# Optimization experiments

Hardware: AMD Instinct MI355X
Metric: run time of the kernel (lower is better)

## Reference

```python
import jax, jax.numpy as jnp
import numpy as np

B, S, D = 2, 2048, 2048
KVH, QPG, HD = 8, 4, 64          # kv heads, q heads per group, head size
THETA = 1024.0
PARTIAL = 0.5
SOFT_CAP = 50.0
EPS = 1e-5


def setup_inputs() -> dict:
    key = jax.random.key(0)
    ks = jax.random.split(key, 8)
    scale = 0.02
    return {
        "x": jax.random.normal(ks[0], (B, S, D), jnp.float32),
        "wq": jax.random.normal(ks[1], (KVH, QPG, HD, D), jnp.float32) * scale,
        "wk": jax.random.normal(ks[2], (KVH, HD, D), jnp.float32) * scale,
        "wv": jax.random.normal(ks[3], (KVH, HD, D), jnp.float32) * scale,
        "wo": jax.random.normal(ks[4], (D, KVH, QPG, HD), jnp.float32) * scale,
        "qn_w": jnp.ones((HD,), jnp.float32),
        "kn_w": jnp.ones((HD,), jnp.float32),
        "pos_ids": jnp.arange(S, dtype=jnp.int32),
    }


def _rms_norm(t, w):
    var = jnp.mean(jnp.square(t), axis=-1, keepdims=True)
    return t * jax.lax.rsqrt(var + EPS) * w


def _rope_tables(pos_ids):
    half = HD // 2
    rotated_size = int(HD * PARTIAL)
    inv_freq = 1.0 / THETA ** (jnp.arange(0, 2 * half, 2, dtype=jnp.float32) / rotated_size)
    inv_freq = jnp.where(jnp.arange(half) < rotated_size // 2, inv_freq, 0.0)
    freqs = pos_ids.astype(jnp.float32)[:, None] * inv_freq[None, :]   # [S, half]
    emb = jnp.concatenate([freqs, freqs], axis=-1)                      # [S, HD]
    return jnp.cos(emb), jnp.sin(emb)


def _apply_rope(t, cos, sin):
    # t: [..., S, HD]; rotate_half: (x1, x2) -> (-x2, x1)
    half = HD // 2
    x1, x2 = t[..., :half], t[..., half:]
    rot = jnp.concatenate([-x2, x1], axis=-1)
    return t * cos + rot * sin


def reference(x, wq, wk, wv, wo, qn_w, kn_w, pos_ids):
    # QKV projections (GQA)
    q = jnp.einsum("bsd,gphd->bgpsh", x, wq)   # [B,KVH,QPG,S,HD]
    k = jnp.einsum("bsd,ghd->bgsh", x, wk)      # [B,KVH,S,HD]
    v = jnp.einsum("bsd,ghd->bgsh", x, wv)

    # QK-norm (RMS over head dim)
    q = _rms_norm(q, qn_w)
    k = _rms_norm(k, kn_w)

    # partial RoPE
    cos, sin = _rope_tables(pos_ids)            # [S, HD]
    q = _apply_rope(q, cos, sin).astype(x.dtype)
    k = _apply_rope(k, cos, sin).astype(x.dtype)

    # attention in fp32 (upcast_attn) with soft cap and causal mask
    scale = 1.0 / jnp.sqrt(jnp.float32(HD))
    scores = jnp.einsum("bgpsh,bgth->bgpst", q.astype(jnp.float32), k.astype(jnp.float32)) * scale
    scores = SOFT_CAP * jnp.tanh(scores / SOFT_CAP)
    causal = pos_ids[:, None] >= pos_ids[None, :]                    # [S, S]
    scores = jnp.where(causal, scores, jnp.finfo(jnp.float32).min)
    probs = jax.nn.softmax(scores, axis=-1)
    attn = jnp.einsum("bgpst,bgth->bgpsh", probs, v.astype(jnp.float32)).astype(x.dtype)

    # output projection (flatten kv_head x q_heads_per_group -> heads)
    out = jnp.einsum("bgpsh,dgph->bsd", attn, wo)
    return out
```

## Files before the change

### kernel.cpp

```cpp
#include <hip/hip_runtime.h>
#include <stdint.h>

#define S_LEN   2048
#define D_MODEL 2048
#define N_KVH   8
#define N_QPG   4
#define N_HD    64

typedef __attribute__((ext_vector_type(8))) short  short8;
typedef __attribute__((ext_vector_type(4))) short  short4v;
typedef __attribute__((ext_vector_type(4))) float  float4v;

__device__ __forceinline__ unsigned short f2bf(float x) {
    unsigned int u = __float_as_uint(x);
    u = (u + 0x7fffu + ((u >> 16) & 1u)) >> 16;
    return (unsigned short)u;
}

__device__ __forceinline__ void gload_lds16(const unsigned short* g, unsigned short* l) {
    __builtin_amdgcn_global_load_lds((const __attribute__((address_space(1))) unsigned int*)g,
                                     (__attribute__((address_space(3))) unsigned int*)l,
                                     16, 0, 0);
}

__device__ __forceinline__ short8 lds_read8(const unsigned short* p) {
    union { short8 s8; short4v s4[2]; } u;
    u.s4[0] = *(const short4v*)p;
    u.s4[1] = *(const short4v*)(p + 4);
    return u.s8;
}

__global__ __launch_bounds__(256) void cvt_all(const float* __restrict__ x,
                                               const float* __restrict__ wq,
                                               const float* __restrict__ wk,
                                               const float* __restrict__ wv,
                                               const float* __restrict__ wo,
                                               unsigned short* __restrict__ xb,
                                               unsigned short* __restrict__ wqb,
                                               unsigned short* __restrict__ wkb,
                                               unsigned short* __restrict__ wvb,
                                               unsigned short* __restrict__ wob) {
    size_t i = (size_t)blockIdx.x * 256 + threadIdx.x;
    const float* src; unsigned short* dst; size_t off;
    if      (i < 1048576) { src = x;  dst = xb;  off = i; }
    else if (i < 1572864) { src = wq; dst = wqb; off = i - 1048576; }
    else if (i < 1703936) { src = wk; dst = wkb; off = i - 1572864; }
    else if (i < 1835008) { src = wv; dst = wvb; off = i - 1703936; }
    else                  { src = wo; dst = wob; off = i - 1835008; }
    const float4* p = (const float4*)src + off * 2;
    float4 a = p[0], b = p[1];
    union { unsigned short us[8]; uint4 v; } u;
    u.us[0] = f2bf(a.x); u.us[1] = f2bf(a.y); u.us[2] = f2bf(a.z); u.us[3] = f2bf(a.w);
    u.us[4] = f2bf(b.x); u.us[5] = f2bf(b.y); u.us[6] = f2bf(b.z); u.us[7] = f2bf(b.w);
    ((uint4*)dst)[off] = u.v;
}

#define EPI_OUT 0
#define EPI_Q   1

template<int EPI>
__global__ __launch_bounds__(256)
void gemm_bt(const unsigned short* __restrict__ A,
             const unsigned short* __restrict__ B,
             void* __restrict__ C,
             const float* __restrict__ normw,
             int M, int N, int K)
{
    __shared__ __align__(16) unsigned short Alds[128 * 32];
    __shared__ __align__(16) unsigned short Blds[128 * 32];

    const int tid  = threadIdx.x;
    const int lane = tid & 63;
    const int wave = tid >> 6;
    const int quad = lane >> 4;
    const int l15  = lane & 15;
    const int m0 = blockIdx.x * 128;
    const int n0 = blockIdx.y * 128;
    const int wm = (wave >> 1) * 64;
    const int wn = (wave & 1) * 64;

    float4v acc[4][4];
#pragma unroll
    for (int i = 0; i < 4; i++)
#pragma unroll
        for (int j = 0; j < 4; j++) acc[i][j] = (float4v){0.f, 0.f, 0.f, 0.f};

    const int j0 = wave * 2;
    const int lr = lane >> 2;
    const int lc = (lane & 3) * 8;
    const unsigned short* Ag = A + (size_t)(m0 + j0 * 16 + lr) * K + lc;
    const unsigned short* Bg = B + (size_t)(n0 + j0 * 16 + lr) * K + lc;
    unsigned short* Al = Alds + j0 * 512;
    unsigned short* Bl = Blds + j0 * 512;

    for (int k0 = 0; k0 < K; k0 += 32) {
        __syncthreads();
        gload_lds16(Ag + k0,          Al);
        gload_lds16(Ag + 16 * K + k0, Al + 512);
        gload_lds16(Bg + k0,          Bl);
        gload_lds16(Bg + 16 * K + k0, Bl + 512);
        __syncthreads();

        short8 af[4], bf[4];
#pragma unroll
        for (int mt = 0; mt < 4; mt++)
            af[mt] = *(const short8*)(Alds + (wm + mt * 16 + l15) * 32 + quad * 8);
#pragma unroll
        for (int nt = 0; nt < 4; nt++)
            bf[nt] = *(const short8*)(Blds + (wn + nt * 16 + l15) * 32 + quad * 8);
#pragma unroll
        for (int mt = 0; mt < 4; mt++)
#pragma unroll
            for (int nt = 0; nt < 4; nt++)
                acc[mt][nt] = __builtin_amdgcn_mfma_f32_16x16x32_bf16(af[mt], bf[nt], acc[mt][nt], 0, 0, 0);
    }

    const int nb = n0 + wn;
#pragma unroll
    for (int mt = 0; mt < 4; mt++) {
#pragma unroll
        for (int r = 0; r < 4; r++) {
            const int m = m0 + wm + mt * 16 + quad * 4 + r;
            if constexpr (EPI == EPI_OUT) {
#pragma unroll
                for (int nt = 0; nt < 4; nt++) {
                    int n = nb + nt * 16 + l15;
                    ((float*)C)[(size_t)m * N + n] = acc[mt][nt][r];
                }
            } else {
                float v0 = acc[mt][0][r], v1 = acc[mt][1][r], v2 = acc[mt][2][r], v3 = acc[mt][3][r];
                float s2 = v0 * v0 + v1 * v1 + v2 * v2 + v3 * v3;
#pragma unroll
                for (int off = 1; off < 16; off <<= 1) s2 += __shfl_xor(s2, off, 64);
                float rs = rsqrtf(s2 * (1.0f / 64.0f) + 1e-5f);
                float nv0 = v0 * rs * normw[0 * 16 + l15];
                float nv1 = v1 * rs * normw[1 * 16 + l15];
                float nv2 = v2 * rs * normw[2 * 16 + l15];
                float nv3 = v3 * rs * normw[3 * 16 + l15];
                const int bidx = m >> 11, s = m & 2047;
                float ang = (float)s * exp2f(-0.625f * (float)l15);
                float sn, cs;
                __sincosf(ang, &sn, &cs);
                float o0 = nv0 * cs - nv2 * sn;
                float o2 = nv2 * cs + nv0 * sn;
                const int g = nb >> 8, p = (nb >> 6) & 3;
                unsigned short* dst = (unsigned short*)C +
                    ((((size_t)bidx * N_KVH + g) * N_QPG + p) * S_LEN + s) * N_HD;
                dst[0 * 16 + l15] = f2bf(o0);
                dst[1 * 16 + l15] = f2bf(nv1);
                dst[2 * 16 + l15] = f2bf(o2);
                dst[3 * 16 + l15] = f2bf(nv3);
            }
        }
    }
}

__global__ __launch_bounds__(256)
void gemm_kv(const unsigned short* __restrict__ xb,
             const unsigned short* __restrict__ wkb,
             const unsigned short* __restrict__ wvb,
             unsigned short* __restrict__ kout,
             unsigned short* __restrict__ vtout,
             const float* __restrict__ knw)
{
    __shared__ __align__(16) unsigned short Alds[128 * 32];
    __shared__ __align__(16) unsigned short Blds[128 * 32];

    const int tid  = threadIdx.x;
    const int lane = tid & 63;
    const int wave = tid >> 6;
    const int quad = lane >> 4;
    const int l15  = lane & 15;
    const int bx = blockIdx.x, by = blockIdx.y;
    const bool isK = (by < 4);
    const unsigned short* A = isK ? xb  : wvb;
    const unsigned short* B = isK ? wkb : xb;
    const int m0 = isK ? bx * 128 : (by - 4) * 128;
    const int n0 = isK ? by * 128 : bx * 128;
    const int K = 2048;
    const int wm = (wave >> 1) * 64;
    const int wn = (wave & 1) * 64;

    float4v acc[4][4];
#pragma unroll
    for (int i = 0; i < 4; i++)
#pragma unroll
        for (int j = 0; j < 4; j++) acc[i][j] = (float4v){0.f, 0.f, 0.f, 0.f};

    const int j0 = wave * 2;
    const int lr = lane >> 2;
    const int lc = (lane & 3) * 8;
    const unsigned short* Ag = A + (size_t)(m0 + j0 * 16 + lr) * K + lc;
    const unsigned short* Bg = B + (size_t)(n0 + j0 * 16 + lr) * K + lc;
    unsigned short* Al = Alds + j0 * 512;
    unsigned short* Bl = Blds + j0 * 512;

    for (int k0 = 0; k0 < K; k0 += 32) {
        __syncthreads();
        gload_lds16(Ag + k0,          Al);
        gload_lds16(Ag + 16 * K + k0, Al + 512);
        gload_lds16(Bg + k0,          Bl);
        gload_lds16(Bg + 16 * K + k0, Bl + 512);
        __syncthreads();

        short8 af[4], bf[4];
#pragma unroll
        for (int mt = 0; mt < 4; mt++)
            af[mt] = *(const short8*)(Alds + (wm + mt * 16 + l15) * 32 + quad * 8);
#pragma unroll
        for (int nt = 0; nt < 4; nt++)
            bf[nt] = *(const short8*)(Blds + (wn + nt * 16 + l15) * 32 + quad * 8);
#pragma unroll
        for (int mt = 0; mt < 4; mt++)
#pragma unroll
            for (int nt = 0; nt < 4; nt++)
                acc[mt][nt] = __builtin_amdgcn_mfma_f32_16x16x32_bf16(af[mt], bf[nt], acc[mt][nt], 0, 0, 0);
    }

    const int nb = n0 + wn;
#pragma unroll
    for (int mt = 0; mt < 4; mt++) {
#pragma unroll
        for (int r = 0; r < 4; r++) {
            const int m = m0 + wm + mt * 16 + quad * 4 + r;
            if (isK) {
                float v0 = acc[mt][0][r], v1 = acc[mt][1][r], v2 = acc[mt][2][r], v3 = acc[mt][3][r];
                float s2 = v0 * v0 + v1 * v1 + v2 * v2 + v3 * v3;
#pragma unroll
                for (int off = 1; off < 16; off <<= 1) s2 += __shfl_xor(s2, off, 64);
                float rs = rsqrtf(s2 * (1.0f / 64.0f) + 1e-5f);
                float nv0 = v0 * rs * knw[0 * 16 + l15];
                float nv1 = v1 * rs * knw[1 * 16 + l15];
                float nv2 = v2 * rs * knw[2 * 16 + l15];
                float nv3 = v3 * rs * knw[3 * 16 + l15];
                const int bidx = m >> 11, s = m & 2047;
                float ang = (float)s * exp2f(-0.625f * (float)l15);
                float sn, cs;
                __sincosf(ang, &sn, &cs);
                float o0 = nv0 * cs - nv2 * sn;
                float o2 = nv2 * cs + nv0 * sn;
                const int g = nb >> 6;
                unsigned short* dst = kout +
                    (((size_t)bidx * N_KVH + g) * S_LEN + s) * N_HD;
                dst[0 * 16 + l15] = f2bf(o0);
                dst[1 * 16 + l15] = f2bf(nv1);
                dst[2 * 16 + l15] = f2bf(o2);
                dst[3 * 16 + l15] = f2bf(nv3);
            } else {
#pragma unroll
                for (int nt = 0; nt < 4; nt++) {
                    int n = nb + nt * 16 + l15;
                    vtout[((size_t)(n >> 11) * 512 + m) * 2048 + (n & 2047)] =
                        f2bf(acc[mt][nt][r]);
                }
            }
        }
    }
}

#define PSTRIDE 68

__global__ __launch_bounds__(256)
void attn_kernel(const unsigned short* __restrict__ Q,
                 const unsigned short* __restrict__ Kb,
                 const unsigned short* __restrict__ Vt,
                 unsigned short* __restrict__ O)
{
    __shared__ __align__(16) unsigned short Kf[8 * 512];
    __shared__ __align__(16) unsigned short Vf[8 * 512];
    __shared__ __align__(16) unsigned short Plds[4 * 32 * PSTRIDE];

    const int tid  = threadIdx.x;
    const int lane = tid & 63;
    const int w    = tid >> 6;
    const int quad = lane >> 4;
    const int l15  = lane & 15;
    const int lhi  = lane >> 4;
    const int qt = 63 - blockIdx.x;
    const int qrow0 = qt * 32;
    const int bg = blockIdx.y;
    const int b = bg >> 3, g = bg & 7;

    const unsigned short* qbase  = Q  + (((size_t)b * N_KVH + g) * N_QPG + w) * S_LEN * N_HD;
    const unsigned short* kbase  = Kb + ((size_t)b * N_KVH + g) * S_LEN * N_HD;
    const unsigned short* vtbase = Vt + ((size_t)b * N_KVH + g) * (size_t)N_HD * S_LEN;

    const unsigned short* sptr[4];
    unsigned short*       ldst[4];
    int                   step[4];
#pragma unroll
    for (int j = 0; j < 4; j++) {
        int ri = w * 4 + j;
        int isV = ri >> 3, rr = ri & 7, nt = rr >> 1, ks = rr & 1;
        if (isV) {
            sptr[j] = vtbase + (size_t)(nt * 16 + l15) * S_LEN + ks * 32 + lhi * 8;
            step[j] = 64;
            ldst[j] = Vf + rr * 512;
        } else {
            sptr[j] = kbase + (size_t)(nt * 16 + l15) * N_HD + ks * 32 + lhi * 8;
            step[j] = 64 * N_HD;
            ldst[j] = Kf + rr * 512;
        }
    }

    unsigned short* Pw = Plds + w * (32 * PSTRIDE);

    short8 qf[2][2];
#pragma unroll
    for (int mt = 0; mt < 2; mt++)
#pragma unroll
        for (int ks = 0; ks < 2; ks++)
            qf[mt][ks] = *(const short8*)(qbase + (size_t)(qrow0 + mt * 16 + l15) * N_HD + ks * 32 + quad * 8);

    float4v o_acc[2][4];
#pragma unroll
    for (int mt = 0; mt < 2; mt++)
#pragma unroll
        for (int nt = 0; nt < 4; nt++) o_acc[mt][nt] = (float4v){0.f, 0.f, 0.f, 0.f};
    float rsum[2][4];
#pragma unroll
    for (int mt = 0; mt < 2; mt++)
#pragma unroll
        for (int r = 0; r < 4; r++) rsum[mt][r] = 0.f;

    const int ktend = qrow0 >> 6;
    for (int kt = 0; kt <= ktend; kt++) {
        __syncthreads();
#pragma unroll
        for (int j = 0; j < 4; j++)
            gload_lds16(sptr[j] + (size_t)kt * step[j], ldst[j]);
        __syncthreads();

        float4v s_acc[2][4];
#pragma unroll
        for (int mt = 0; mt < 2; mt++)
#pragma unroll
            for (int nt = 0; nt < 4; nt++) s_acc[mt][nt] = (float4v){0.f, 0.f, 0.f, 0.f};
#pragma unroll
        for (int ks = 0; ks < 2; ks++) {
            short8 kfr[4];
#pragma unroll
            for (int nt = 0; nt < 4; nt++)
                kfr[nt] = *(const short8*)(Kf + (nt * 2 + ks) * 512 + lane * 8);
#pragma unroll
            for (int mt = 0; mt < 2; mt++)
#pragma unroll
                for (int nt = 0; nt < 4; nt++)
                    s_acc[mt][nt] = __builtin_amdgcn_mfma_f32_16x16x32_bf16(qf[mt][ks], kfr[nt], s_acc[mt][nt], 0, 0, 0);
        }

        const bool diag = (kt == ktend);
#pragma unroll
        for (int mt = 0; mt < 2; mt++) {
#pragma unroll
            for (int r = 0; r < 4; r++) {
                const int s_q  = qrow0 + mt * 16 + quad * 4 + r;
                const int prow = (mt * 16 + quad * 4 + r) * PSTRIDE;
#pragma unroll
                for (int nt = 0; nt < 4; nt++) {
                    float a = s_acc[mt][nt][r];
                    float z = a * 2.5e-3f;
                    float t = fmaf(z * z, -0.33333334f, 1.0f);
                    float p = __builtin_amdgcn_exp2f(
                        fmaf(a * 0.18033688f, t, -72.13475204f));
                    if (diag) {
                        int s_k = kt * 64 + nt * 16 + l15;
                        p = (s_k <= s_q) ? p : 0.0f;
                    }
                    rsum[mt][r] += p;
                    Pw[prow + nt * 16 + l15] =
                        (unsigned short)((__float_as_uint(p) + 0x8000u) >> 16);
                }
            }
        }

#pragma unroll
        for (int ks = 0; ks < 2; ks++) {
            short8 pf[2], vfr[4];
#pragma unroll
            for (int mt = 0; mt < 2; mt++)
                pf[mt] = lds_read8(Pw + (mt * 16 + l15) * PSTRIDE + ks * 32 + quad * 8);
#pragma unroll
            for (int nt = 0; nt < 4; nt++)
                vfr[nt] = *(const short8*)(Vf + (nt * 2 + ks) * 512 + lane * 8);
#pragma unroll
            for (int mt = 0; mt < 2; mt++)
#pragma unroll
                for (int nt = 0; nt < 4; nt++)
                    o_acc[mt][nt] = __builtin_amdgcn_mfma_f32_16x16x32_bf16(pf[mt], vfr[nt], o_acc[mt][nt], 0, 0, 0);
        }
    }

#pragma unroll
    for (int mt = 0; mt < 2; mt++) {
#pragma unroll
        for (int r = 0; r < 4; r++) {
            float s = rsum[mt][r];
            s += __shfl_xor(s, 1, 64);
            s += __shfl_xor(s, 2, 64);
            s += __shfl_xor(s, 4, 64);
            s += __shfl_xor(s, 8, 64);
            float inv = 1.0f / s;
            int s_q = qrow0 + mt * 16 + quad * 4 + r;
            size_t rowoff = ((size_t)(b * S_LEN + s_q)) * D_MODEL + (g * N_QPG + w) * N_HD;
#pragma unroll
            for (int nt = 0; nt < 4; nt++)
                O[rowoff + nt * 16 + l15] = f2bf(o_acc[mt][nt][r] * inv);
        }
    }
}

extern "C" void kernel_launch(void* const* d_in, const int* in_sizes, int n_in,
                              void* d_out, int out_size, void* d_ws, size_t ws_size,
                              hipStream_t stream)
{
    const float* x    = (const float*)d_in[0];
    const float* wq   = (const float*)d_in[1];
    const float* wk   = (const float*)d_in[2];
    const float* wv   = (const float*)d_in[3];
    const float* wo   = (const float*)d_in[4];
    const float* qn_w = (const float*)d_in[5];
    const float* kn_w = (const float*)d_in[6];

    char* ws = (char*)d_ws;
    unsigned short* xb  = (unsigned short*)(ws + 0);
    unsigned short* wqb = (unsigned short*)(ws + 16777216);
    unsigned short* wkb = (unsigned short*)(ws + 25165824);
    unsigned short* wvb = (unsigned short*)(ws + 27262976);
    unsigned short* wob = (unsigned short*)(ws + 29360128);
    unsigned short* qb  = (unsigned short*)(ws + 37748736);
    unsigned short* kb  = (unsigned short*)(ws + 54525952);
    unsigned short* vt  = (unsigned short*)(ws + 58720256);
    unsigned short* ab  = (unsigned short*)(ws + 62914560);

    cvt_all<<<dim3(9216), 256, 0, stream>>>(x, wq, wk, wv, wo, xb, wqb, wkb, wvb, wob);

    gemm_bt<EPI_Q><<<dim3(32, 16), 256, 0, stream>>>(xb, wqb, qb, qn_w, 4096, 2048, 2048);
    gemm_kv<<<dim3(32, 8), 256, 0, stream>>>(xb, wkb, wvb, kb, vt, kn_w);

    attn_kernel<<<dim3(64, 16), 256, 0, stream>>>(qb, kb, vt, ab);

    gemm_bt<EPI_OUT><<<dim3(32, 16), 256, 0, stream>>>(ab, wob, d_out, nullptr, 4096, 2048, 2048);
}
```

Baseline: 420.3 us.

## Pair causal query tiles per block and load K/V directly into registers

Each attention block now handles two query tiles, qx and 63-qx, so the causal work per block is balanced, and the grid is halved. The shared-memory K/V staging and its two block barriers per step are removed. Each wave now loads K and V fragments straight from global memory into registers and prefetches the next K tile. The soft-cap polynomial is refactored into one fewer multiply. The trade-off is that all four waves load the same K/V redundantly from global/L2 with no sharing through LDS, and register pressure rises.

```diff
diff --git a/kernel.cpp b/kernel.cpp
--- a/kernel.cpp
+++ b/kernel.cpp
@@ -266,8 +266,6 @@
                  const unsigned short* __restrict__ Vt,
                  unsigned short* __restrict__ O)
 {
-    __shared__ __align__(16) unsigned short Kf[8 * 512];
-    __shared__ __align__(16) unsigned short Vf[8 * 512];
     __shared__ __align__(16) unsigned short Plds[4 * 32 * PSTRIDE];
 
     const int tid  = threadIdx.x;
@@ -275,9 +273,7 @@
     const int w    = tid >> 6;
     const int quad = lane >> 4;
     const int l15  = lane & 15;
-    const int lhi  = lane >> 4;
-    const int qt = 63 - blockIdx.x;
-    const int qrow0 = qt * 32;
+    const int qx = blockIdx.x;
     const int bg = blockIdx.y;
     const int b = bg >> 3, g = bg & 7;
 
@@ -285,127 +281,122 @@
     const unsigned short* kbase  = Kb + ((size_t)b * N_KVH + g) * S_LEN * N_HD;
     const unsigned short* vtbase = Vt + ((size_t)b * N_KVH + g) * (size_t)N_HD * S_LEN;
 
-    const unsigned short* sptr[4];
-    unsigned short*       ldst[4];
-    int                   step[4];
-#pragma unroll
-    for (int j = 0; j < 4; j++) {
-        int ri = w * 4 + j;
-        int isV = ri >> 3, rr = ri & 7, nt = rr >> 1, ks = rr & 1;
-        if (isV) {
-            sptr[j] = vtbase + (size_t)(nt * 16 + l15) * S_LEN + ks * 32 + lhi * 8;
-            step[j] = 64;
-            ldst[j] = Vf + rr * 512;
-        } else {
-            sptr[j] = kbase + (size_t)(nt * 16 + l15) * N_HD + ks * 32 + lhi * 8;
-            step[j] = 64 * N_HD;
-            ldst[j] = Kf + rr * 512;
+    unsigned short* Pw = Plds + w * (32 * PSTRIDE);
+
+    for (int half = 0; half < 2; half++) {
+        const int qt = half ? (63 - qx) : qx;
+        const int qrow0 = qt * 32;
+
+        short8 qf[2][2];
+#pragma unroll
+        for (int mt = 0; mt < 2; mt++)
+#pragma unroll
+            for (int ks = 0; ks < 2; ks++)
+                qf[mt][ks] = *(const short8*)(qbase + (size_t)(qrow0 + mt * 16 + l15) * N_HD + ks * 32 + quad * 8);
+
+        float4v o_acc[2][4];
+#pragma unroll
+        for (int mt = 0; mt < 2; mt++)
+#pragma unroll
+            for (int nt = 0; nt < 4; nt++) o_acc[mt][nt] = (float4v){0.f, 0.f, 0.f, 0.f};
+        float rsum[2][4];
+#pragma unroll
+        for (int mt = 0; mt < 2; mt++)
+#pragma unroll
+            for (int r = 0; r < 4; r++) rsum[mt][r] = 0.f;
+
+        const int ktend = qrow0 >> 6;
+
+        short8 kf[4][2];
+#pragma unroll
+        for (int nt = 0; nt < 4; nt++)
+#pragma unroll
+            for (int ks = 0; ks < 2; ks++)
+                kf[nt][ks] = *(const short8*)(kbase + (size_t)(nt * 16 + l15) * N_HD + ks * 32 + quad * 8);
+
+        for (int kt = 0; kt <= ktend; kt++) {
+            float4v s_acc[2][4];
+#pragma unroll
+            for (int mt = 0; mt < 2; mt++)
+#pragma unroll
+                for (int nt = 0; nt < 4; nt++) s_acc[mt][nt] = (float4v){0.f, 0.f, 0.f, 0.f};
+#pragma unroll
+            for (int ks = 0; ks < 2; ks++)
+#pragma unroll
+                for (int mt = 0; mt < 2; mt++)
+#pragma unroll
+                    for (int nt = 0; nt < 4; nt++)
+                        s_acc[mt][nt] = __builtin_amdgcn_mfma_f32_16x16x32_bf16(qf[mt][ks], kf[nt][ks], s_acc[mt][nt], 0, 0, 0);
+
+            short8 vf[4][2];
+#pragma unroll
+            for (int nt = 0; nt < 4; nt++)
+#pragma unroll
+                for (int ks = 0; ks < 2; ks++)
+                    vf[nt][ks] = *(const short8*)(vtbase + (size_t)(nt * 16 + l15) * S_LEN + kt * 64 + ks * 32 + quad * 8);
+
+            if (kt < ktend) {
+#pragma unroll
+                for (int nt = 0; nt < 4; nt++)
+#pragma unroll
+                    for (int ks = 0; ks < 2; ks++)
+                        kf[nt][ks] = *(const short8*)(kbase + (size_t)((kt + 1) * 64 + nt * 16 + l15) * N_HD + ks * 32 + quad * 8);
+            }
+
+            const bool diag = (kt == ktend);
+#pragma unroll
+            for (int mt = 0; mt < 2; mt++) {
+#pragma unroll
+                for (int r = 0; r < 4; r++) {
+                    const int s_q  = qrow0 + mt * 16 + quad * 4 + r;
+                    const int prow = (mt * 16 + quad * 4 + r) * PSTRIDE;
+#pragma unroll
+                    for (int nt = 0; nt < 4; nt++) {
+                        float a = s_acc[mt][nt][r];
+                        float u = a * a;
+                        float wv = fmaf(u, -3.757018e-7f, 0.18033688f);
+                        float p = __builtin_amdgcn_exp2f(fmaf(a, wv, -72.13475204f));
+                        if (diag) {
+                            int s_k = kt * 64 + nt * 16 + l15;
+                            p = (s_k <= s_q) ? p : 0.0f;
+                        }
+                        rsum[mt][r] += p;
+                        Pw[prow + nt * 16 + l15] =
+                            (unsigned short)((__float_as_uint(p) + 0x8000u) >> 16);
+                    }
+                }
+            }
+
+#pragma unroll
+            for (int ks = 0; ks < 2; ks++) {
+                short8 pf[2];
+#pragma unroll
+                for (int mt = 0; mt < 2; mt++)
+                    pf[mt] = lds_read8(Pw + (mt * 16 + l15) * PSTRIDE + ks * 32 + quad * 8);
+#pragma unroll
+                for (int mt = 0; mt < 2; mt++)
+#pragma unroll
+                    for (int nt = 0; nt < 4; nt++)
+                        o_acc[mt][nt] = __builtin_amdgcn_mfma_f32_16x16x32_bf16(pf[mt], vf[nt][ks], o_acc[mt][nt], 0, 0, 0);
+            }
         }
-    }
-
-    unsigned short* Pw = Plds + w * (32 * PSTRIDE);
-
-    short8 qf[2][2];
-#pragma unroll
-    for (int mt = 0; mt < 2; mt++)
-#pragma unroll
-        for (int ks = 0; ks < 2; ks++)
-            qf[mt][ks] = *(const short8*)(qbase + (size_t)(qrow0 + mt * 16 + l15) * N_HD + ks * 32 + quad * 8);
-
-    float4v o_acc[2][4];
-#pragma unroll
-    for (int mt = 0; mt < 2; mt++)
-#pragma unroll
-        for (int nt = 0; nt < 4; nt++) o_acc[mt][nt] = (float4v){0.f, 0.f, 0.f, 0.f};
-    float rsum[2][4];
-#pragma unroll
-    for (int mt = 0; mt < 2; mt++)
-#pragma unroll
-        for (int r = 0; r < 4; r++) rsum[mt][r] = 0.f;
-
-    const int ktend = qrow0 >> 6;
-    for (int kt = 0; kt <= ktend; kt++) {
-        __syncthreads();
-#pragma unroll
-        for (int j = 0; j < 4; j++)
-            gload_lds16(sptr[j] + (size_t)kt * step[j], ldst[j]);
-        __syncthreads();
-
-        float4v s_acc[2][4];
-#pragma unroll
-        for (int mt = 0; mt < 2; mt++)
-#pragma unroll
-            for (int nt = 0; nt < 4; nt++) s_acc[mt][nt] = (float4v){0.f, 0.f, 0.f, 0.f};
-#pragma unroll
-        for (int ks = 0; ks < 2; ks++) {
-            short8 kfr[4];
-#pragma unroll
-            for (int nt = 0; nt < 4; nt++)
-                kfr[nt] = *(const short8*)(Kf + (nt * 2 + ks) * 512 + lane * 8);
-#pragma unroll
-            for (int mt = 0; mt < 2; mt++)
+
+#pragma unroll
+        for (int mt = 0; mt < 2; mt++) {
+#pragma unroll
+            for (int r = 0; r < 4; r++) {
+                float s = rsum[mt][r];
+                s += __shfl_xor(s, 1, 64);
+                s += __shfl_xor(s, 2, 64);
+                s += __shfl_xor(s, 4, 64);
+                s += __shfl_xor(s, 8, 64);
+                float inv = 1.0f / s;
+                int s_q = qrow0 + mt * 16 + quad * 4 + r;
+                size_t rowoff = ((size_t)(b * S_LEN + s_q)) * D_MODEL + (g * N_QPG + w) * N_HD;
 #pragma unroll
                 for (int nt = 0; nt < 4; nt++)
-                    s_acc[mt][nt] = __builtin_amdgcn_mfma_f32_16x16x32_bf16(qf[mt][ks], kfr[nt], s_acc[mt][nt], 0, 0, 0);
-        }
-
-        const bool diag = (kt == ktend);
-#pragma unroll
-        for (int mt = 0; mt < 2; mt++) {
-#pragma unroll
-            for (int r = 0; r < 4; r++) {
-                const int s_q  = qrow0 + mt * 16 + quad * 4 + r;
-                const int prow = (mt * 16 + quad * 4 + r) * PSTRIDE;
-#pragma unroll
-                for (int nt = 0; nt < 4; nt++) {
-                    float a = s_acc[mt][nt][r];
-                    float z = a * 2.5e-3f;
-                    float t = fmaf(z * z, -0.33333334f, 1.0f);
-                    float p = __builtin_amdgcn_exp2f(
-                        fmaf(a * 0.18033688f, t, -72.13475204f));
-                    if (diag) {
-                        int s_k = kt * 64 + nt * 16 + l15;
-                        p = (s_k <= s_q) ? p : 0.0f;
-                    }
-                    rsum[mt][r] += p;
-                    Pw[prow + nt * 16 + l15] =
-                        (unsigned short)((__float_as_uint(p) + 0x8000u) >> 16);
-                }
-            }
-        }
-
-#pragma unroll
-        for (int ks = 0; ks < 2; ks++) {
-            short8 pf[2], vfr[4];
-#pragma unroll
-            for (int mt = 0; mt < 2; mt++)
-                pf[mt] = lds_read8(Pw + (mt * 16 + l15) * PSTRIDE + ks * 32 + quad * 8);
-#pragma unroll
-            for (int nt = 0; nt < 4; nt++)
-                vfr[nt] = *(const short8*)(Vf + (nt * 2 + ks) * 512 + lane * 8);
-#pragma unroll
-            for (int mt = 0; mt < 2; mt++)
-#pragma unroll
-                for (int nt = 0; nt < 4; nt++)
-                    o_acc[mt][nt] = __builtin_amdgcn_mfma_f32_16x16x32_bf16(pf[mt], vfr[nt], o_acc[mt][nt], 0, 0, 0);
-        }
-    }
-
-#pragma unroll
-    for (int mt = 0; mt < 2; mt++) {
-#pragma unroll
-        for (int r = 0; r < 4; r++) {
-            float s = rsum[mt][r];
-            s += __shfl_xor(s, 1, 64);
-            s += __shfl_xor(s, 2, 64);
-            s += __shfl_xor(s, 4, 64);
-            s += __shfl_xor(s, 8, 64);
-            float inv = 1.0f / s;
-            int s_q = qrow0 + mt * 16 + quad * 4 + r;
-            size_t rowoff = ((size_t)(b * S_LEN + s_q)) * D_MODEL + (g * N_QPG + w) * N_HD;
-#pragma unroll
-            for (int nt = 0; nt < 4; nt++)
-                O[rowoff + nt * 16 + l15] = f2bf(o_acc[mt][nt][r] * inv);
+                    O[rowoff + nt * 16 + l15] = f2bf(o_acc[mt][nt][r] * inv);
+            }
         }
     }
 }
@@ -438,7 +429,7 @@
     gemm_bt<EPI_Q><<<dim3(32, 16), 256, 0, stream>>>(xb, wqb, qb, qn_w, 4096, 2048, 2048);
     gemm_kv<<<dim3(32, 8), 256, 0, stream>>>(xb, wkb, wvb, kb, vt, kn_w);
 
-    attn_kernel<<<dim3(64, 16), 256, 0, stream>>>(qb, kb, vt, ab);
+    attn_kernel<<<dim3(32, 16), 256, 0, stream>>>(qb, kb, vt, ab);
 
     gemm_bt<EPI_OUT><<<dim3(32, 16), 256, 0, stream>>>(ab, wob, d_out, nullptr, 4096, 2048, 2048);
 }
```

Result: faster. 391.0 us (-7.0%).
